# Performance work log

Measured on AMD Instinct MI355X. Metric: run time of the kernel, lower is better.

The kernel has to match this reference:

```python
import jax, jax.numpy as jnp
import numpy as np

N_NODES = 100000
N_EDGES = 1000000
N_GRAPHS = 4096
F_IN = 9
H = 64


def setup_inputs() -> dict:
    key = jax.random.key(0)
    ks = jax.random.split(key, 12)
    x = jax.random.normal(ks[0], (N_NODES, F_IN), dtype=jnp.float32)
    edge_index = jax.random.randint(ks[1], (2, N_EDGES), 0, N_NODES, dtype=jnp.int64)
    batch = jnp.sort(jax.random.randint(ks[2], (N_NODES,), 0, N_GRAPHS, dtype=jnp.int64))
    def lin(k, fan_in, fan_out):
        s = 1.0 / np.sqrt(fan_in)
        return jax.random.uniform(k, (fan_in, fan_out), jnp.float32, -s, s)
    return {
        "x": x, "edge_index": edge_index, "batch": batch,
        "W1": lin(ks[3], F_IN, H), "b1": jnp.zeros((H,), jnp.float32),
        "W2": lin(ks[4], H, H),    "b2": jnp.zeros((H,), jnp.float32),
        "W3": lin(ks[5], H, H),    "b3": jnp.zeros((H,), jnp.float32),
        "W4": lin(ks[6], H, H),    "b4": jnp.zeros((H,), jnp.float32),
        "Wout": lin(ks[7], H, 1),  "bout": jnp.zeros((1,), jnp.float32),
    }


def reference(x, edge_index, batch, W1, b1, W2, b2, W3, b3, W4, b4, Wout, bout):
    N = x.shape[0]
    loops = jnp.arange(N, dtype=edge_index.dtype)
    src = jnp.concatenate([edge_index[0], loops])  # messages flow src -> dst (PyG source_to_target)
    dst = jnp.concatenate([edge_index[1], loops])
    # symmetric GCN normalization with self-loops: deg includes self-loop
    deg = jax.ops.segment_sum(jnp.ones_like(dst, dtype=x.dtype), dst, num_segments=N)
    dis = jax.lax.rsqrt(jnp.maximum(deg, 1.0))  # deg >= 1 thanks to self-loops
    norm = dis[src] * dis[dst]                  # [E+N]

    def gcn_conv(h, W, b):
        h = h @ W                                # transform first (PyG order)
        msgs = h[src] * norm[:, None]            # [E+N, H]
        return jax.ops.segment_sum(msgs, dst, num_segments=N) + b

    h = jax.nn.relu(gcn_conv(x, W1, b1))
    h = jax.nn.relu(gcn_conv(h, W2, b2))
    h = jax.nn.relu(gcn_conv(h, W3, b3))
    h = jax.nn.relu(gcn_conv(h, W4, b4))

    # global mean pool over graphs
    sums = jax.ops.segment_sum(h, batch, num_segments=N_GRAPHS)      # [G, H]
    counts = jax.ops.segment_sum(jnp.ones((N,), h.dtype), batch, num_segments=N_GRAPHS)
    pooled = sums / jnp.maximum(counts, 1.0)[:, None]
    return pooled @ Wout + bout                  # [G, 1]
```

## Files before the change

kernel.cpp:

```cpp
#include <hip/hip_runtime.h>
#include <hip/hip_fp16.h>


static inline size_t align256(size_t x){ return (x + 255) & ~size_t(255); }

#define CHUNK 2048

struct __align__(8)  h4v { __half2 a, b; };
struct __align__(16) h8v { __half2 a, b, c, d; };

typedef _Float16 f16x8 __attribute__((ext_vector_type(8)));
typedef float    f32x4 __attribute__((ext_vector_type(4)));

__global__ void k_zero(float* gsum, int G){
  int i = blockIdx.x*blockDim.x + threadIdx.x;
  if (i < G) gsum[i] = 0.f;
}

__global__ __launch_bounds__(256) void k_sortchunk(
    const int* __restrict__ src, const int* __restrict__ dst,
    int* __restrict__ binned, int* __restrict__ hoffC, int E){
  __shared__ int hcnt[1024];
  __shared__ int simg[CHUNK];
  int c = blockIdx.x, t = threadIdx.x;
  int e0 = c*CHUNK;
  int cnt = E - e0; if (cnt > CHUNK) cnt = CHUNK;

  for (int i = t; i < 1024; i += 256) hcnt[i] = 0;
  __syncthreads();

  int b_[8], r_[8], v_[8];
  #pragma unroll
  for (int j = 0; j < 8; j++){
    int i = t + j*256;
    if (i < cnt){
      int d = dst[e0+i];
      int s = src[e0+i];
      int b = d >> 7;
      b_[j] = b;
      r_[j] = atomicAdd(&hcnt[b], 1);
      v_[j] = (s << 7) | (d & 127);
    } else b_[j] = -1;
  }
  __syncthreads();

  int own[4];
  #pragma unroll
  for (int j = 0; j < 4; j++) own[j] = hcnt[t + j*256];
  for (int off = 1; off < 1024; off <<= 1){
    int nv[4];
    #pragma unroll
    for (int j = 0; j < 4; j++){
      int i = t + j*256;
      nv[j] = hcnt[i] + ((i >= off) ? hcnt[i-off] : 0);
    }
    __syncthreads();
    #pragma unroll
    for (int j = 0; j < 4; j++) hcnt[t + j*256] = nv[j];
    __syncthreads();
  }
  #pragma unroll
  for (int j = 0; j < 4; j++) hcnt[t + j*256] -= own[j];
  __syncthreads();

  for (int i = t; i < 783; i += 256) hoffC[c*783 + i] = hcnt[i];

  #pragma unroll
  for (int j = 0; j < 8; j++)
    if (b_[j] >= 0) simg[hcnt[b_[j]] + r_[j]] = v_[j];
  __syncthreads();

  for (int i = t; i < cnt; i += 256) binned[e0 + i] = simg[i];
}

__global__ __launch_bounds__(256) void k_bktsum(
    const int* __restrict__ hoffC, int* __restrict__ btot, int NC, int NBK){
  __shared__ int s[256];
  int b = blockIdx.x, t = threadIdx.x;
  int tot = 0;
  for (int c = t; c < NC; c += 256)
    tot += hoffC[c*783 + b + 1] - hoffC[c*783 + b];
  s[t] = tot; __syncthreads();
  for (int off = 128; off > 0; off >>= 1){
    if (t < off) s[t] += s[t+off];
    __syncthreads();
  }
  if (t == 0) btot[b] = s[0];
}

__global__ __launch_bounds__(1024) void k_bktscan(
    const int* __restrict__ btot, int* __restrict__ bbase,
    int* __restrict__ row_ptr, int NBK, int N, int E){
  __shared__ int s[1024];
  int t = threadIdx.x;
  int v = (t < NBK) ? btot[t] : 0;
  s[t] = v; __syncthreads();
  for (int off = 1; off < 1024; off <<= 1){
    int add = (t >= off) ? s[t-off] : 0; __syncthreads();
    s[t] += add; __syncthreads();
  }
  if (t < NBK) bbase[t] = s[t] - v;
  if (t == 0) row_ptr[N] = E;
}

__global__ __launch_bounds__(256) void k_gather2(
    const int* __restrict__ binned, const int* __restrict__ hoffC,
    const int* __restrict__ bbase,
    int* __restrict__ row_ptr, float* __restrict__ dis,
    int* __restrict__ csr, int N, int NC){
  __shared__ int lcur[128];
  __shared__ int lscan[128];
  int b = blockIdx.x, t = threadIdx.x;
  int n0 = b << 7;
  int nn = N - n0; if (nn > 128) nn = 128;
  if (t < 128) lcur[t] = 0;
  __syncthreads();
  for (int c = t; c < NC; c += 256){
    int o0 = hoffC[c*783 + b];
    int o1 = hoffC[c*783 + b + 1];
    int base = c*CHUNK;
    for (int k = o0; k < o1; k++)
      atomicAdd(&lcur[binned[base + k] & 127], 1);
  }
  __syncthreads();
  int degv = (t < 128) ? lcur[t] : 0;
  if (t < 128) lscan[t] = degv;
  __syncthreads();
  for (int off = 1; off < 128; off <<= 1){
    int add = (t < 128 && t >= off) ? lscan[t-off] : 0;
    __syncthreads();
    if (t < 128) lscan[t] += add;
    __syncthreads();
  }
  int bb = bbase[b];
  if (t < nn){
    int row = bb + lscan[t] - degv;
    row_ptr[n0 + t] = row;
    dis[n0 + t] = rsqrtf((float)(degv + 1));
    lcur[t] = row;
  }
  __syncthreads();
  for (int c = t; c < NC; c += 256){
    int o0 = hoffC[c*783 + b];
    int o1 = hoffC[c*783 + b + 1];
    int base = c*CHUNK;
    for (int k = o0; k < o1; k++){
      int v = binned[base + k];
      int pos = atomicAdd(&lcur[v & 127], 1);
      csr[pos] = v >> 7;
    }
  }
}

__global__ void k_premul(const float* __restrict__ x, const float* __restrict__ dis,
                         float* __restrict__ xs, int N){
  int i = blockIdx.x*blockDim.x + threadIdx.x;
  if (i < N*9) xs[i] = x[i]*dis[i/9];
}

__global__ void k_agg9(const float* __restrict__ xs, const float* __restrict__ dis,
                       const int* __restrict__ row_ptr, const int* __restrict__ csr,
                       float* __restrict__ xagg, int N){
  int tid = blockIdx.x*blockDim.x + threadIdx.x;
  if (tid >= N*9) return;
  int n = tid/9, f = tid - n*9;
  float dn = dis[n];
  int s0 = row_ptr[n], s1 = row_ptr[n+1];
  float a0 = xs[tid];
  float a1 = 0.f, a2 = 0.f, a3 = 0.f;
  int j = s0;
  for (; j + 3 < s1; j += 4){
    int e0 = csr[j], e1 = csr[j+1], e2 = csr[j+2], e3 = csr[j+3];
    a0 += xs[e0*9+f];
    a1 += xs[e1*9+f];
    a2 += xs[e2*9+f];
    a3 += xs[e3*9+f];
  }
  for (; j < s1; j++) a0 += xs[csr[j]*9+f];
  xagg[tid] = ((a0+a1)+(a2+a3))*dn;
}

__device__ __forceinline__ void mfma_epilogue(
    const _Float16* hlw, const f16x8 (&wf)[4][2],
    __half* __restrict__ mo, int wid, int nwaves, int N, int lane){
  int lm = lane & 15, lk = lane >> 4;
  f16x8 hb0 = *(const f16x8*)(hlw + lm*72 + lk*8);
  f16x8 hb1 = *(const f16x8*)(hlw + lm*72 + 32 + lk*8);
  int node = wid + lm*nwaves;
  bool ok = (node < N);
  __half* row = mo + (size_t)node*64;
  #pragma unroll
  for (int ft = 0; ft < 4; ft++){
    f32x4 acc = {0.f, 0.f, 0.f, 0.f};
    acc = __builtin_amdgcn_mfma_f32_16x16x32_f16(wf[ft][0], hb0, acc, 0, 0, 0);
    acc = __builtin_amdgcn_mfma_f32_16x16x32_f16(wf[ft][1], hb1, acc, 0, 0, 0);
    if (ok){
      h4v o;
      o.a = __floats2half2_rn(acc[0], acc[1]);
      o.b = __floats2half2_rn(acc[2], acc[3]);
      *(h4v*)(row + ft*16 + lk*4) = o;
    }
  }
}

#define LOAD_WFRAGS(Wn)                                                    \
  f16x8 wf[4][2];                                                          \
  { int lm_ = lane & 15, lk_ = lane >> 4;                                  \
    _Pragma("unroll") for (int ft = 0; ft < 4; ft++)                       \
    _Pragma("unroll") for (int kb = 0; kb < 2; kb++)                       \
    _Pragma("unroll") for (int j = 0; j < 8; j++)                          \
      wf[ft][kb][j] = (_Float16)Wn[(kb*32 + lk_*8 + j)*64 + ft*16 + lm_]; }

__global__ __launch_bounds__(256) void k_lin1_fused(
    const float* __restrict__ xagg, const float* __restrict__ W1,
    const float* __restrict__ b1, const float* __restrict__ dis,
    const float* __restrict__ W2, __half* __restrict__ mo, int N, int nwaves){
  __shared__ float W1l[576];
  __shared__ float b1l[64];
  __shared__ _Float16 hl[4][16*72];
  int t = threadIdx.x;
  for (int i = t; i < 576; i += 256) W1l[i] = W1[i];
  if (t < 64) b1l[t] = b1[t];
  __syncthreads();
  int lane = t & 63, w = t >> 6;
  int wid = (blockIdx.x*blockDim.x + t) >> 6;
  LOAD_WFRAGS(W2)
  _Float16* hlw = hl[w];
  for (int i = 0; i < 16; i++){
    int n = wid + i*nwaves;
    _Float16 hv = (_Float16)0.f;
    if (n < N){
      float acc = b1l[lane];
      #pragma unroll
      for (int k = 0; k < 9; k++) acc = fmaf(xagg[n*9+k], W1l[k*64+lane], acc);
      hv = (_Float16)(fmaxf(acc, 0.f) * dis[n]);
    }
    hlw[i*72 + lane] = hv;
  }
  mfma_epilogue(hlw, wf, mo, wid, nwaves, N, lane);
}

#define ACC8(g_)  do{ float2 t_;                                   \
  t_ = __half22float2((g_).a); acc0 += t_.x; acc1 += t_.y;         \
  t_ = __half22float2((g_).b); acc2 += t_.x; acc3 += t_.y;         \
  t_ = __half22float2((g_).c); acc4 += t_.x; acc5 += t_.y;         \
  t_ = __half22float2((g_).d); acc6 += t_.x; acc7 += t_.y; }while(0)

#define RED3(v)  do{ v += __shfl_xor(v, 8,64);                     \
                     v += __shfl_xor(v,16,64);                     \
                     v += __shfl_xor(v,32,64); }while(0)

#define AGG_ISSUE(n_, rp0_, rp1_, rn0_, rn1_, e0_, e1_, g0_, g1_, sf_, dn_) \
  do{                                                                      \
    int nn_ = (n_) + 2*nwaves;                                             \
    rn0_ = 0; rn1_ = 0;                                                    \
    if (nn_ < N){ rn0_ = row_ptr[nn_]; rn1_ = row_ptr[nn_+1]; }            \
    e0_ = -1; e1_ = -1;                                                    \
    if ((n_) < N){                                                         \
      sf_ = m[(size_t)(n_)*8 + q2];                                        \
      dn_ = dis[n_];                                                       \
      int j0_ = (rp0_) + sub, j1_ = (rp0_) + 8 + sub;                      \
      if (j0_ < (rp1_)) e0_ = csr[j0_];                                    \
      if (j1_ < (rp1_)) e1_ = csr[j1_];                                    \
      if (e0_ >= 0) g0_ = m[(size_t)e0_*8 + q2];                           \
      if (e1_ >= 0) g1_ = m[(size_t)e1_*8 + q2];                           \
    }                                                                      \
  }while(0)

#define AGG_ACCRED(n_, rp0_, rp1_, e0_, e1_, g0_, g1_, sf_, dn_)           \
      float acc0=0.f,acc1=0.f,acc2=0.f,acc3=0.f;                           \
      float acc4=0.f,acc5=0.f,acc6=0.f,acc7=0.f;                           \
      if (e0_ >= 0) ACC8(g0_);                                             \
      if (e1_ >= 0) ACC8(g1_);                                             \
      for (int j_ = (rp0_) + 16 + sub; j_ < (rp1_); j_ += 8){              \
        h8v gx_ = m[(size_t)csr[j_]*8 + q2]; ACC8(gx_);                    \
      }                                                                    \
      RED3(acc0); RED3(acc1); RED3(acc2); RED3(acc3);                      \
      RED3(acc4); RED3(acc5); RED3(acc6); RED3(acc7);                      \
      float2 s01=__half22float2((sf_).a), s23=__half22float2((sf_).b);     \
      float2 s45=__half22float2((sf_).c), s67=__half22float2((sf_).d);     \
      float r0 = fmaxf(fmaf(acc0 + s01.x, dn_, bb0.x), 0.f);               \
      float r1 = fmaxf(fmaf(acc1 + s01.y, dn_, bb0.y), 0.f);               \
      float r2 = fmaxf(fmaf(acc2 + s23.x, dn_, bb0.z), 0.f);               \
      float r3 = fmaxf(fmaf(acc3 + s23.y, dn_, bb0.w), 0.f);               \
      float r4 = fmaxf(fmaf(acc4 + s45.x, dn_, bb1.x), 0.f);               \
      float r5 = fmaxf(fmaf(acc5 + s45.y, dn_, bb1.y), 0.f);               \
      float r6 = fmaxf(fmaf(acc6 + s67.x, dn_, bb1.z), 0.f);               \
      float r7 = fmaxf(fmaf(acc7 + s67.y, dn_, bb1.w), 0.f);

#define AGG_REDUCE(n_, rp0_, rp1_, e0_, e1_, g0_, g1_, sf_, dn_, i_)       \
  do{                                                                      \
    if ((n_) < N){                                                         \
      AGG_ACCRED(n_, rp0_, rp1_, e0_, e1_, g0_, g1_, sf_, dn_)             \
      if (sub == 0){                                                       \
        h8v hv_;                                                           \
        hv_.a = __floats2half2_rn(r0*(dn_), r1*(dn_));                     \
        hv_.b = __floats2half2_rn(r2*(dn_), r3*(dn_));                     \
        hv_.c = __floats2half2_rn(r4*(dn_), r5*(dn_));                     \
        hv_.d = __floats2half2_rn(r6*(dn_), r7*(dn_));                     \
        *(h8v*)(hlw + (i_)*72 + q2*8) = hv_;                               \
      }                                                                    \
    } else if (sub == 0){                                                  \
      h8v z_; z_.a = __floats2half2_rn(0.f, 0.f);                          \
      z_.b = z_.a; z_.c = z_.a; z_.d = z_.a;                               \
      *(h8v*)(hlw + (i_)*72 + q2*8) = z_;                                  \
    }                                                                      \
  }while(0)

__global__ __launch_bounds__(256) void k_agg_fused(
    const h8v* __restrict__ m, const float* __restrict__ dis,
    const float* __restrict__ b, const float* __restrict__ Wn,
    const int* __restrict__ row_ptr, const int* __restrict__ csr,
    __half* __restrict__ mo, int N, int nwaves){
  __shared__ _Float16 hl[4][16*72];
  int t = threadIdx.x;
  int lane = t & 63, w = t >> 6;
  int sub = lane >> 3, q2 = lane & 7;
  int wid = (blockIdx.x*blockDim.x + t) >> 6;
  _Float16* hlw = hl[w];
  const float4* b4 = (const float4*)b;
  float4 bb0 = b4[q2*2], bb1 = b4[q2*2+1];

  int nA = wid,          rA0 = 0, rA1 = 0;
  int nB = wid + nwaves, rB0 = 0, rB1 = 0;
  if (nA < N){ rA0 = row_ptr[nA]; rA1 = row_ptr[nA+1]; }
  if (nB < N){ rB0 = row_ptr[nB]; rB1 = row_ptr[nB+1]; }
  int eA0, eA1, eB0, eB1, rnA0, rnA1, rnB0, rnB1;
  h8v gA0, gA1, sfA, gB0, gB1, sfB;
  float dnA = 0.f, dnB = 0.f;
  AGG_ISSUE(nA, rA0, rA1, rnA0, rnA1, eA0, eA1, gA0, gA1, sfA, dnA);
  for (int p = 0; p < 8; p++){
    AGG_ISSUE(nB, rB0, rB1, rnB0, rnB1, eB0, eB1, gB0, gB1, sfB, dnB);
    AGG_REDUCE(nA, rA0, rA1, eA0, eA1, gA0, gA1, sfA, dnA, 2*p);
    nA += 2*nwaves; rA0 = rnA0; rA1 = rnA1;
    if (p < 7)
      AGG_ISSUE(nA, rA0, rA1, rnA0, rnA1, eA0, eA1, gA0, gA1, sfA, dnA);
    AGG_REDUCE(nB, rB0, rB1, eB0, eB1, gB0, gB1, sfB, dnB, 2*p+1);
    nB += 2*nwaves; rB0 = rnB0; rB1 = rnB1;
  }
  LOAD_WFRAGS(Wn)
  mfma_epilogue(hlw, wf, mo, wid, nwaves, N, lane);
}

__global__ __launch_bounds__(256) void k_agg64_out(
    const h8v* __restrict__ m, const float* __restrict__ dis,
    const float* __restrict__ b, const float* __restrict__ Wout,
    const int* __restrict__ batch,
    const int* __restrict__ row_ptr, const int* __restrict__ csr,
    float* gsum, int N, int nwaves){
  int lane = threadIdx.x & 63;
  int sub = lane >> 3, q2 = lane & 7;
  int n = (blockIdx.x*blockDim.x + threadIdx.x) >> 6;
  if (n >= N) return;
  int rp0 = row_ptr[n], rp1 = row_ptr[n+1];
  const float4* b4 = (const float4*)b;
  const float4* wo4 = (const float4*)Wout;
  while (true){
    int nn = n + nwaves;
    int np0 = 0, np1 = 0;
    if (nn < N){ np0 = row_ptr[nn]; np1 = row_ptr[nn+1]; }
    h8v sf = m[(size_t)n*8 + q2];
    float dn = dis[n];
    int bg = batch[n];
    float acc0=0.f,acc1=0.f,acc2=0.f,acc3=0.f,acc4=0.f,acc5=0.f,acc6=0.f,acc7=0.f;
    int s1 = rp1;
    int j0 = rp0 + sub, j1 = rp0 + 8 + sub;
    if (j0 < s1){ h8v a = m[(size_t)csr[j0]*8 + q2]; ACC8(a); }
    if (j1 < s1){ h8v a = m[(size_t)csr[j1]*8 + q2]; ACC8(a); }
    for (int j = rp0 + 16 + sub; j < s1; j += 8){
      h8v a = m[(size_t)csr[j]*8 + q2]; ACC8(a);
    }
    RED3(acc0); RED3(acc1); RED3(acc2); RED3(acc3);
    RED3(acc4); RED3(acc5); RED3(acc6); RED3(acc7);
    float2 s01 = __half22float2(sf.a), s23 = __half22float2(sf.b);
    float2 s45 = __half22float2(sf.c), s67 = __half22float2(sf.d);
    float4 bb0 = b4[q2*2], bb1 = b4[q2*2+1];
    float4 w0 = wo4[q2*2], w1 = wo4[q2*2+1];
    float r0 = fmaxf(fmaf(acc0 + s01.x, dn, bb0.x), 0.f);
    float r1 = fmaxf(fmaf(acc1 + s01.y, dn, bb0.y), 0.f);
    float r2 = fmaxf(fmaf(acc2 + s23.x, dn, bb0.z), 0.f);
    float r3 = fmaxf(fmaf(acc3 + s23.y, dn, bb0.w), 0.f);
    float r4 = fmaxf(fmaf(acc4 + s45.x, dn, bb1.x), 0.f);
    float r5 = fmaxf(fmaf(acc5 + s45.y, dn, bb1.y), 0.f);
    float r6 = fmaxf(fmaf(acc6 + s67.x, dn, bb1.z), 0.f);
    float r7 = fmaxf(fmaf(acc7 + s67.y, dn, bb1.w), 0.f);
    float p = r0*w0.x + r1*w0.y + r2*w0.z + r3*w0.w
            + r4*w1.x + r5*w1.y + r6*w1.z + r7*w1.w;
    p += __shfl_xor(p,1,64); p += __shfl_xor(p,2,64); p += __shfl_xor(p,4,64);
    if (lane == 0) atomicAdd(&gsum[bg], p);
    if (nn >= N) break;
    n = nn; rp0 = np0; rp1 = np1;
  }
}

__global__ void k_final(const float* __restrict__ gsum, const int* __restrict__ batch,
                        const float* __restrict__ bout, float* __restrict__ out,
                        int G, int N){
  int g = blockIdx.x*blockDim.x + threadIdx.x;
  if (g >= G) return;
  int lo = 0, hi = N;
  while (lo < hi){ int mid = (lo+hi)>>1; if (batch[mid] <  g) lo = mid+1; else hi = mid; }
  int lb = lo;
  lo = 0; hi = N;
  while (lo < hi){ int mid = (lo+hi)>>1; if (batch[mid] <= g) lo = mid+1; else hi = mid; }
  int c = lo - lb;
  out[g] = gsum[g]/(float)(c > 0 ? c : 1) + bout[0];
}

extern "C" void kernel_launch(void* const* d_in, const int* in_sizes, int n_in,
                              void* d_out, int out_size, void* d_ws, size_t ws_size,
                              hipStream_t stream){
  const float* x    = (const float*)d_in[0];
  const int*   ei   = (const int*)d_in[1];
  const int*   batch= (const int*)d_in[2];
  const float* W1 = (const float*)d_in[3];  const float* b1 = (const float*)d_in[4];
  const float* W2 = (const float*)d_in[5];  const float* b2 = (const float*)d_in[6];
  const float* W3 = (const float*)d_in[7];  const float* b3 = (const float*)d_in[8];
  const float* W4 = (const float*)d_in[9];  const float* b4 = (const float*)d_in[10];
  const float* Wout = (const float*)d_in[11]; const float* bout = (const float*)d_in[12];
  float* out = (float*)d_out;

  const int N = in_sizes[0]/9;
  const int E = in_sizes[1]/2;
  const int G = out_size;
  const int* src = ei;
  const int* dst = ei + E;

  char* ws = (char*)d_ws;
  size_t off = 0;
  auto alloc = [&](size_t bytes){ void* p = ws + off; off = align256(off + bytes); return p; };
  int*   row_ptr  = (int*)  alloc((size_t)(N+1)*4);
  int*   csr      = (int*)  alloc((size_t)E*4);
  float* dis      = (float*)alloc((size_t)N*4);
  const int NBK = (N + 127)/128;
  const int NC  = (E + CHUNK-1)/CHUNK;
  int*   hoffC    = (int*)  alloc((size_t)NC*783*4);
  int*   btot     = (int*)  alloc((size_t)NBK*4);
  int*   bbase    = (int*)  alloc((size_t)NBK*4);
  float* gsum     = (float*)alloc((size_t)G*4);
  __half* mA      = (__half*)alloc((size_t)N*64*2);
  __half* mB      = (__half*)alloc((size_t)N*64*2);
  int*   binned   = (int*)mA;
  float* xs       = (float*)mB;
  float* xagg     = xs + (size_t)N*9;

  const int AGG_BLOCKS = 2048;
  const int AGG_WAVES  = AGG_BLOCKS*4;

  k_zero     <<<(G+255)/256, 256, 0, stream>>>(gsum, G);
  k_sortchunk<<<NC, 256, 0, stream>>>(src, dst, binned, hoffC, E);
  k_bktsum   <<<NBK, 256, 0, stream>>>(hoffC, btot, NC, NBK);
  k_bktscan  <<<1, 1024, 0, stream>>>(btot, bbase, row_ptr, NBK, N, E);
  k_gather2  <<<NBK, 256, 0, stream>>>(binned, hoffC, bbase, row_ptr, dis, csr, N, NC);

  k_premul<<<(N*9+255)/256, 256, 0, stream>>>(x, dis, xs, N);
  k_agg9  <<<(N*9+255)/256, 256, 0, stream>>>(xs, dis, row_ptr, csr, xagg, N);
  k_lin1_fused<<<AGG_BLOCKS, 256, 0, stream>>>(xagg, W1, b1, dis, W2, mA, N, AGG_WAVES);

  k_agg_fused<<<AGG_BLOCKS, 256, 0, stream>>>((const h8v*)mA, dis, b2, W3,
                                              row_ptr, csr, mB, N, AGG_WAVES);
  k_agg_fused<<<AGG_BLOCKS, 256, 0, stream>>>((const h8v*)mB, dis, b3, W4,
                                              row_ptr, csr, mA, N, AGG_WAVES);
  k_agg64_out<<<AGG_BLOCKS, 256, 0, stream>>>((const h8v*)mA, dis, b4, Wout, batch,
                                              row_ptr, csr, gsum, N, AGG_WAVES);

  k_final<<<(G+255)/256, 256, 0, stream>>>(gsum, batch, bout, out, G, N);
}
```

Measured before the change: 308.2 us.

## Fuse zeroing and premul into CSR build, stage bucket edges, pipeline output aggregation

Folds the gsum zeroing into k_bktsum and the x*dis premultiply into k_gather2, removing two kernel launches. k_gather2 now stages each bucket's binned edges in shared memory during the counting pass, so the scatter pass reads them from LDS instead of re-reading global binned data, with a fallback when the staged count exceeds capacity. The final aggregation kernel is software-pipelined over two nodes, issuing loads for the next node before reducing the current one. This costs more shared memory and registers, and the staging adds an extra shared atomic per chunk, which may lower occupancy.

```diff
diff --git a/kernel.cpp b/kernel.cpp
--- a/kernel.cpp
+++ b/kernel.cpp
@@ -5,17 +5,13 @@
 static inline size_t align256(size_t x){ return (x + 255) & ~size_t(255); }
 
 #define CHUNK 2048
+#define SCAP  3072
 
 struct __align__(8)  h4v { __half2 a, b; };
 struct __align__(16) h8v { __half2 a, b, c, d; };
 
 typedef _Float16 f16x8 __attribute__((ext_vector_type(8)));
 typedef float    f32x4 __attribute__((ext_vector_type(4)));
-
-__global__ void k_zero(float* gsum, int G){
-  int i = blockIdx.x*blockDim.x + threadIdx.x;
-  if (i < G) gsum[i] = 0.f;
-}
 
 __global__ __launch_bounds__(256) void k_sortchunk(
     const int* __restrict__ src, const int* __restrict__ dst,
@@ -74,9 +70,12 @@
 }
 
 __global__ __launch_bounds__(256) void k_bktsum(
-    const int* __restrict__ hoffC, int* __restrict__ btot, int NC, int NBK){
+    const int* __restrict__ hoffC, int* __restrict__ btot,
+    float* __restrict__ gsum, int NC, int NBK, int G){
   __shared__ int s[256];
   int b = blockIdx.x, t = threadIdx.x;
+  int gid = b*256 + t;
+  if (gid < G) gsum[gid] = 0.f;
   int tot = 0;
   for (int c = t; c < NC; c += 256)
     tot += hoffC[c*783 + b + 1] - hoffC[c*783 + b];
@@ -105,22 +104,34 @@
 
 __global__ __launch_bounds__(256) void k_gather2(
     const int* __restrict__ binned, const int* __restrict__ hoffC,
-    const int* __restrict__ bbase,
+    const int* __restrict__ bbase, const float* __restrict__ x,
     int* __restrict__ row_ptr, float* __restrict__ dis,
-    int* __restrict__ csr, int N, int NC){
+    float* __restrict__ xs, int* __restrict__ csr, int N, int NC){
   __shared__ int lcur[128];
   __shared__ int lscan[128];
+  __shared__ float ldis[128];
+  __shared__ int stage[SCAP];
+  __shared__ int scount;
   int b = blockIdx.x, t = threadIdx.x;
   int n0 = b << 7;
   int nn = N - n0; if (nn > 128) nn = 128;
   if (t < 128) lcur[t] = 0;
+  if (t == 0) scount = 0;
   __syncthreads();
   for (int c = t; c < NC; c += 256){
     int o0 = hoffC[c*783 + b];
     int o1 = hoffC[c*783 + b + 1];
-    int base = c*CHUNK;
-    for (int k = o0; k < o1; k++)
-      atomicAdd(&lcur[binned[base + k] & 127], 1);
+    int len = o1 - o0;
+    if (len > 0){
+      int base = atomicAdd(&scount, len);
+      int sbase = c*CHUNK;
+      for (int k = 0; k < len; k++){
+        int v = binned[sbase + o0 + k];
+        atomicAdd(&lcur[v & 127], 1);
+        int pos = base + k;
+        if (pos < SCAP) stage[pos] = v;
+      }
+    }
   }
   __syncthreads();
   int degv = (t < 128) ? lcur[t] : 0;
@@ -136,26 +147,33 @@
   if (t < nn){
     int row = bb + lscan[t] - degv;
     row_ptr[n0 + t] = row;
-    dis[n0 + t] = rsqrtf((float)(degv + 1));
+    float dv = rsqrtf((float)(degv + 1));
+    dis[n0 + t] = dv;
+    ldis[t] = dv;
     lcur[t] = row;
   }
   __syncthreads();
-  for (int c = t; c < NC; c += 256){
-    int o0 = hoffC[c*783 + b];
-    int o1 = hoffC[c*783 + b + 1];
-    int base = c*CHUNK;
-    for (int k = o0; k < o1; k++){
-      int v = binned[base + k];
+  for (int i = t; i < nn*9; i += 256)
+    xs[(size_t)n0*9 + i] = x[(size_t)n0*9 + i] * ldis[i/9];
+  int sc = scount;
+  if (sc <= SCAP){
+    for (int i = t; i < sc; i += 256){
+      int v = stage[i];
       int pos = atomicAdd(&lcur[v & 127], 1);
       csr[pos] = v >> 7;
     }
-  }
-}
-
-__global__ void k_premul(const float* __restrict__ x, const float* __restrict__ dis,
-                         float* __restrict__ xs, int N){
-  int i = blockIdx.x*blockDim.x + threadIdx.x;
-  if (i < N*9) xs[i] = x[i]*dis[i/9];
+  } else {
+    for (int c = t; c < NC; c += 256){
+      int o0 = hoffC[c*783 + b];
+      int o1 = hoffC[c*783 + b + 1];
+      int sbase = c*CHUNK;
+      for (int k = o0; k < o1; k++){
+        int v = binned[sbase + k];
+        int pos = atomicAdd(&lcur[v & 127], 1);
+        csr[pos] = v >> 7;
+      }
+    }
+  }
 }
 
 __global__ void k_agg9(const float* __restrict__ xs, const float* __restrict__ dis,
@@ -307,6 +325,34 @@
     }                                                                      \
   }while(0)
 
+#define OUT_ISSUE(n_, rp0_, rp1_, rn0_, rn1_, e0_, e1_, g0_, g1_, sf_, dn_, bg_) \
+  do{                                                                      \
+    int pn_ = (n_) + nwaves;                                               \
+    rn0_ = 0; rn1_ = 0;                                                    \
+    if (pn_ < N){ rn0_ = row_ptr[pn_]; rn1_ = row_ptr[pn_+1]; }            \
+    sf_ = m[(size_t)(n_)*8 + q2];                                          \
+    dn_ = dis[n_];                                                         \
+    bg_ = batch[n_];                                                       \
+    e0_ = -1; e1_ = -1;                                                    \
+    int j0_ = (rp0_) + sub, j1_ = (rp0_) + 8 + sub;                        \
+    if (j0_ < (rp1_)) e0_ = csr[j0_];                                      \
+    if (j1_ < (rp1_)) e1_ = csr[j1_];                                      \
+    if (e0_ >= 0) g0_ = m[(size_t)e0_*8 + q2];                             \
+    if (e1_ >= 0) g1_ = m[(size_t)e1_*8 + q2];                             \
+  }while(0)
+
+#define OUT_REDUCE(n_, rp0_, rp1_, e0_, e1_, g0_, g1_, sf_, dn_, bg_)      \
+  do{                                                                      \
+    float4 bb0 = b4[q2*2], bb1 = b4[q2*2+1];                               \
+    float4 w0 = wo4[q2*2], w1 = wo4[q2*2+1];                               \
+    AGG_ACCRED(n_, rp0_, rp1_, e0_, e1_, g0_, g1_, sf_, dn_)               \
+    float p_ = r0*w0.x + r1*w0.y + r2*w0.z + r3*w0.w                       \
+             + r4*w1.x + r5*w1.y + r6*w1.z + r7*w1.w;                      \
+    p_ += __shfl_xor(p_,1,64); p_ += __shfl_xor(p_,2,64);                  \
+    p_ += __shfl_xor(p_,4,64);                                             \
+    if (lane == 0) atomicAdd(&gsum[bg_], p_);                              \
+  }while(0)
+
 __global__ __launch_bounds__(256) void k_agg_fused(
     const h8v* __restrict__ m, const float* __restrict__ dis,
     const float* __restrict__ b, const float* __restrict__ Wn,
@@ -350,46 +396,35 @@
     float* gsum, int N, int nwaves){
   int lane = threadIdx.x & 63;
   int sub = lane >> 3, q2 = lane & 7;
-  int n = (blockIdx.x*blockDim.x + threadIdx.x) >> 6;
-  if (n >= N) return;
-  int rp0 = row_ptr[n], rp1 = row_ptr[n+1];
+  int wid = (blockIdx.x*blockDim.x + threadIdx.x) >> 6;
+  if (wid >= N) return;
   const float4* b4 = (const float4*)b;
   const float4* wo4 = (const float4*)Wout;
-  while (true){
-    int nn = n + nwaves;
-    int np0 = 0, np1 = 0;
-    if (nn < N){ np0 = row_ptr[nn]; np1 = row_ptr[nn+1]; }
-    h8v sf = m[(size_t)n*8 + q2];
-    float dn = dis[n];
-    int bg = batch[n];
-    float acc0=0.f,acc1=0.f,acc2=0.f,acc3=0.f,acc4=0.f,acc5=0.f,acc6=0.f,acc7=0.f;
-    int s1 = rp1;
-    int j0 = rp0 + sub, j1 = rp0 + 8 + sub;
-    if (j0 < s1){ h8v a = m[(size_t)csr[j0]*8 + q2]; ACC8(a); }
-    if (j1 < s1){ h8v a = m[(size_t)csr[j1]*8 + q2]; ACC8(a); }
-    for (int j = rp0 + 16 + sub; j < s1; j += 8){
-      h8v a = m[(size_t)csr[j]*8 + q2]; ACC8(a);
-    }
-    RED3(acc0); RED3(acc1); RED3(acc2); RED3(acc3);
-    RED3(acc4); RED3(acc5); RED3(acc6); RED3(acc7);
-    float2 s01 = __half22float2(sf.a), s23 = __half22float2(sf.b);
-    float2 s45 = __half22float2(sf.c), s67 = __half22float2(sf.d);
-    float4 bb0 = b4[q2*2], bb1 = b4[q2*2+1];
-    float4 w0 = wo4[q2*2], w1 = wo4[q2*2+1];
-    float r0 = fmaxf(fmaf(acc0 + s01.x, dn, bb0.x), 0.f);
-    float r1 = fmaxf(fmaf(acc1 + s01.y, dn, bb0.y), 0.f);
-    float r2 = fmaxf(fmaf(acc2 + s23.x, dn, bb0.z), 0.f);
-    float r3 = fmaxf(fmaf(acc3 + s23.y, dn, bb0.w), 0.f);
-    float r4 = fmaxf(fmaf(acc4 + s45.x, dn, bb1.x), 0.f);
-    float r5 = fmaxf(fmaf(acc5 + s45.y, dn, bb1.y), 0.f);
-    float r6 = fmaxf(fmaf(acc6 + s67.x, dn, bb1.z), 0.f);
-    float r7 = fmaxf(fmaf(acc7 + s67.y, dn, bb1.w), 0.f);
-    float p = r0*w0.x + r1*w0.y + r2*w0.z + r3*w0.w
-            + r4*w1.x + r5*w1.y + r6*w1.z + r7*w1.w;
-    p += __shfl_xor(p,1,64); p += __shfl_xor(p,2,64); p += __shfl_xor(p,4,64);
-    if (lane == 0) atomicAdd(&gsum[bg], p);
-    if (nn >= N) break;
-    n = nn; rp0 = np0; rp1 = np1;
+
+  int nA = wid;
+  int rA0 = row_ptr[nA], rA1 = row_ptr[nA+1];
+  int rnA0, rnA1, rnB0, rnB1;
+  int eA0, eA1, eB0, eB1, bgA, bgB;
+  h8v gA0, gA1, sfA, gB0, gB1, sfB;
+  float dnA, dnB;
+  int rB0, rB1;
+  OUT_ISSUE(nA, rA0, rA1, rnA0, rnA1, eA0, eA1, gA0, gA1, sfA, dnA, bgA);
+  for(;;){
+    int nB = nA + nwaves;
+    if (nB < N){
+      rB0 = rnA0; rB1 = rnA1;
+      OUT_ISSUE(nB, rB0, rB1, rnB0, rnB1, eB0, eB1, gB0, gB1, sfB, dnB, bgB);
+    }
+    OUT_REDUCE(nA, rA0, rA1, eA0, eA1, gA0, gA1, sfA, dnA, bgA);
+    if (nB >= N) return;
+    int nA2 = nB + nwaves;
+    if (nA2 < N){
+      nA = nA2;
+      rA0 = rnB0; rA1 = rnB1;
+      OUT_ISSUE(nA, rA0, rA1, rnA0, rnA1, eA0, eA1, gA0, gA1, sfA, dnA, bgA);
+    }
+    OUT_REDUCE(nB, rB0, rB1, eB0, eB1, gB0, gB1, sfB, dnB, bgB);
+    if (nA2 >= N) return;
   }
 }
 
@@ -447,13 +482,12 @@
   const int AGG_BLOCKS = 2048;
   const int AGG_WAVES  = AGG_BLOCKS*4;
 
-  k_zero     <<<(G+255)/256, 256, 0, stream>>>(gsum, G);
   k_sortchunk<<<NC, 256, 0, stream>>>(src, dst, binned, hoffC, E);
-  k_bktsum   <<<NBK, 256, 0, stream>>>(hoffC, btot, NC, NBK);
+  k_bktsum   <<<NBK, 256, 0, stream>>>(hoffC, btot, gsum, NC, NBK, G);
   k_bktscan  <<<1, 1024, 0, stream>>>(btot, bbase, row_ptr, NBK, N, E);
-  k_gather2  <<<NBK, 256, 0, stream>>>(binned, hoffC, bbase, row_ptr, dis, csr, N, NC);
-
-  k_premul<<<(N*9+255)/256, 256, 0, stream>>>(x, dis, xs, N);
+  k_gather2  <<<NBK, 256, 0, stream>>>(binned, hoffC, bbase, x,
+                                       row_ptr, dis, xs, csr, N, NC);
+
   k_agg9  <<<(N*9+255)/256, 256, 0, stream>>>(xs, dis, row_ptr, csr, xagg, N);
   k_lin1_fused<<<AGG_BLOCKS, 256, 0, stream>>>(xagg, W1, b1, dis, W2, mA, N, AGG_WAVES);
 
```

New measurement: 301.9 us. -2.0%, faster.
